# Kernel tuning notes

Hardware: AMD Instinct MI355X
Metric: run time of the kernel (lower is better)

Reference implementation:

```python
import jax, jax.numpy as jnp
import numpy as np

HIDDEN = 2048
HEADS = 16
HEAD_DIM = HIDDEN // HEADS
ROPE_BASE = 10000.0


def rope_cos_sin(seq_len, dim, dtype=jnp.float32):
    inv_freq = 1.0 / (ROPE_BASE ** (jnp.arange(0, dim, 2, dtype=jnp.float32) / dim))
    t = jnp.arange(seq_len, dtype=jnp.float32)
    freqs = jnp.einsum('i,j->ij', t, inv_freq)            # [S, dim/2]
    emb = jnp.concatenate([freqs, freqs], axis=-1)        # [S, dim]
    return jnp.cos(emb).astype(dtype), jnp.sin(emb).astype(dtype)


def rotate_half(x):
    x1, x2 = jnp.split(x, 2, axis=-1)
    return jnp.concatenate([-x2, x1], axis=-1)


def setup_inputs() -> dict:
    key = jax.random.key(0)
    ks = jax.random.split(key, 6)
    B, S, D = 2, 2048, HIDDEN
    scale = 1.0 / np.sqrt(D)
    x = jax.random.normal(ks[0], (B, S, D), dtype=jnp.float32)
    Wq = jax.random.normal(ks[1], (D, D), dtype=jnp.float32) * scale
    Wk = jax.random.normal(ks[2], (D, D), dtype=jnp.float32) * scale
    Wv = jax.random.normal(ks[3], (D, D), dtype=jnp.float32) * scale
    Wo = jax.random.normal(ks[4], (D, D), dtype=jnp.float32) * scale
    bo = jnp.zeros((D,), dtype=jnp.float32)
    return {"x": x, "Wq": Wq, "Wk": Wk, "Wv": Wv, "Wo": Wo, "bo": bo}


def reference(x, Wq, Wk, Wv, Wo, bo):
    B, S, D = x.shape
    H, Dh = HEADS, HEAD_DIM
    # torch Linear: x @ W.T
    q = (x @ Wq.T).reshape(B, S, H, Dh).transpose(0, 2, 1, 3)  # [B,H,S,Dh]
    k = (x @ Wk.T).reshape(B, S, H, Dh).transpose(0, 2, 1, 3)
    v = (x @ Wv.T).reshape(B, S, H, Dh).transpose(0, 2, 1, 3)
    cos, sin = rope_cos_sin(S, Dh, x.dtype)                    # [S, Dh]
    q = q * cos + rotate_half(q) * sin
    k = k * cos + rotate_half(k) * sin
    scale = Dh ** -0.5
    attn = jnp.einsum('bhqd,bhkd->bhqk', q, k) * scale
    attn = jax.nn.softmax(attn, axis=-1)
    out = jnp.einsum('bhqk,bhkd->bhqd', attn, v)               # [B,H,S,Dh]
    out = out.transpose(0, 2, 1, 3).reshape(B, S, D)
    return out @ Wo.T + bo
```

## Files before the change

kernel.cpp:

```cpp
#include <hip/hip_runtime.h>
#include <stdint.h>


#define SEQ 2048
#define HD 128
#define DMODEL 2048

typedef __bf16 bf16x8 __attribute__((ext_vector_type(8)));
typedef float f32x4 __attribute__((ext_vector_type(4)));
typedef unsigned short u16;
typedef unsigned int u32;

typedef bf16x8 __attribute__((may_alias)) bf16x8_a;
typedef uint2 __attribute__((may_alias)) uint2_a;
typedef uint4 __attribute__((may_alias)) uint4_a;

__device__ __forceinline__ u16 f2bf(float f) {
  unsigned int u = __float_as_uint(f);
  u += 0x7fff + ((u >> 16) & 1);
  return (u16)(u >> 16);
}

typedef __attribute__((address_space(1))) void* gas_t;
typedef __attribute__((address_space(3))) void* las_t;
__device__ __forceinline__ void load_lds16(const void* g, void* l) {
  __builtin_amdgcn_global_load_lds((gas_t)(uintptr_t)g,
                                   (las_t)(uint32_t)(uintptr_t)l, 16, 0, 0);
}

__global__ void conv_all(const float* __restrict__ x,
                         const float* __restrict__ wq,
                         const float* __restrict__ wk,
                         const float* __restrict__ wv,
                         const float* __restrict__ wo,
                         u16* __restrict__ xb, u16* __restrict__ wqkv,
                         u16* __restrict__ wob) {
  int i = blockIdx.x * 256 + threadIdx.x;
  const float* src;
  u16* dst;
  int off;
  if (i < 2097152) { src = x; dst = xb; off = i; }
  else if (i < 3145728) { src = wq; dst = wqkv; off = i - 2097152; }
  else if (i < 4194304) { src = wk; dst = wqkv + 4194304; off = i - 3145728; }
  else if (i < 5242880) { src = wv; dst = wqkv + 8388608; off = i - 4194304; }
  else { src = wo; dst = wob; off = i - 5242880; }
  float4 v = ((const float4*)src)[off];
  ushort4 o;
  o.x = f2bf(v.x); o.y = f2bf(v.y); o.z = f2bf(v.z); o.w = f2bf(v.w);
  ((ushort4*)dst)[off] = o;
}

template <bool SWAP>
__device__ __forceinline__ void gemm_core(
    const u16* __restrict__ A, const u16* __restrict__ Bm, int row0, int col0,
    int K, u16* Asl, u16* Bsl, int wave, int lane, int quad, int l15,
    int waveM, int waveN, f32x4 acc[4][4]) {
  for (int k0 = 0; k0 < K; k0 += 64) {
    __syncthreads();
#pragma unroll
    for (int j = 0; j < 4; ++j) {
      int idx = (wave * 4 + j) * 64 + lane;
      int r = idx >> 3;
      int c8 = (idx & 7) ^ (r & 7);
      load_lds16(A + (size_t)(row0 + r) * K + (k0 + c8 * 8), &Asl[idx * 8]);
      load_lds16(Bm + (size_t)(col0 + r) * K + (k0 + c8 * 8), &Bsl[idx * 8]);
    }
    __syncthreads();
#pragma unroll
    for (int c = 0; c < 2; ++c) {
      bf16x8 af[4], bfr[4];
#pragma unroll
      for (int mt = 0; mt < 4; ++mt) {
        int r = waveM + mt * 16 + l15;
        af[mt] = *(const bf16x8*)&Asl[(r * 8 + ((c * 4 + quad) ^ (r & 7))) * 8];
      }
#pragma unroll
      for (int nt = 0; nt < 4; ++nt) {
        int r = waveN + nt * 16 + l15;
        bfr[nt] = *(const bf16x8*)&Bsl[(r * 8 + ((c * 4 + quad) ^ (r & 7))) * 8];
      }
#pragma unroll
      for (int mt = 0; mt < 4; ++mt)
#pragma unroll
        for (int nt = 0; nt < 4; ++nt) {
          if (SWAP)
            acc[mt][nt] = __builtin_amdgcn_mfma_f32_16x16x32_bf16(
                bfr[nt], af[mt], acc[mt][nt], 0, 0, 0);
          else
            acc[mt][nt] = __builtin_amdgcn_mfma_f32_16x16x32_bf16(
                af[mt], bfr[nt], acc[mt][nt], 0, 0, 0);
        }
    }
  }
}

__global__ __launch_bounds__(256, 3)
void gemm_qkv(const u16* __restrict__ A, const u16* __restrict__ Bm,
              u16* __restrict__ qkv, u16* __restrict__ vt, int K) {
  __shared__ __align__(16) u16 Smem[2][128 * 64];
  u16* Asl = Smem[0];
  u16* Bsl = Smem[1];
  const int tid = threadIdx.x;
  const int lane = tid & 63;
  const int wave = tid >> 6;
  const int quad = lane >> 4;
  const int l15 = lane & 15;
  const int row0 = blockIdx.y * 128;
  const int col0 = blockIdx.x * 128;
  const int waveM = (wave & 1) * 64;
  const int waveN = (wave >> 1) * 64;
  const bool vmode = blockIdx.x >= 32;

  f32x4 acc[4][4] = {};
  if (vmode)
    gemm_core<true>(A, Bm, row0, col0, K, Asl, Bsl, wave, lane, quad, l15,
                    waveM, waveN, acc);
  else
    gemm_core<false>(A, Bm, row0, col0, K, Asl, Bsl, wave, lane, quad, l15,
                     waveM, waveN, acc);

  const int which = col0 >> 11;
  const int h = (col0 >> 7) & 15;
  const int brow = row0 >> 11;
  const int sbase = row0 & 2047;
  const float qs = (which == 0) ? 0.12751744f : 1.0f;

  __syncthreads();
  u16* tile = &Smem[0][0];
#pragma unroll
  for (int mt = 0; mt < 4; ++mt) {
#pragma unroll
    for (int nt = 0; nt < 4; ++nt) {
#pragma unroll
      for (int r = 0; r < 4; ++r) {
        int dd, ss, el;
        if (vmode) {
          dd = waveN + nt * 16 + quad * 4 + r;
          ss = waveM + mt * 16 + l15;
          el = dd * 128 + (((ss >> 3) ^ (dd & 15)) * 8) + (ss & 7);
        } else {
          dd = waveN + nt * 16 + l15;
          ss = waveM + mt * 16 + quad * 4 + r;
          el = ss * 128 + (((dd >> 3) ^ (ss & 15)) * 8) + (dd & 7);
        }
        tile[el] = f2bf(acc[mt][nt][r] * qs);
      }
    }
  }
  __syncthreads();

  const int a = lane & 7;
  const int sg = lane >> 3;
  if (!vmode) {
    const float c1 = 0.2076205059304601f;
    const float c2 = 2.6514961294723187f;
#pragma unroll
    for (int pass = 0; pass < 4; ++pass) {
      int s_l = pass * 32 + wave * 8 + sg;
      int sw = s_l & 15;
      bf16x8 x1 = *(const bf16x8_a*)&tile[s_l * 128 + ((a ^ sw) * 8)];
      bf16x8 x2 = *(const bf16x8_a*)&tile[s_l * 128 + (((a + 8) ^ sw) * 8)];
      int s2048 = sbase + s_l;
      u16 o1[8], o2[8];
#pragma unroll
      for (int e = 0; e < 8; ++e) {
        float j = (float)(a * 8 + e);
        float rev = (float)s2048 * __builtin_amdgcn_exp2f(-c1 * j - c2);
        rev = __builtin_amdgcn_fractf(rev);
        float sn = __builtin_amdgcn_sinf(rev);
        float cs = __builtin_amdgcn_cosf(rev);
        float v1 = (float)x1[e], v2 = (float)x2[e];
        o1[e] = f2bf(v1 * cs - v2 * sn);
        o2[e] = f2bf(v2 * cs + v1 * sn);
      }
      size_t base =
          ((((size_t)which * 2 + brow) * 16 + h) * SEQ + s2048) * HD + a * 8;
      *(uint4_a*)&qkv[base] = *(uint4*)o1;
      *(uint4_a*)&qkv[base + 64] = *(uint4*)o2;
    }
  } else {
#pragma unroll
    for (int pass = 0; pass < 4; ++pass) {
      int d_l = pass * 32 + wave * 8 + sg;
      int dw = d_l & 15;
      bf16x8 y1 = *(const bf16x8_a*)&tile[d_l * 128 + ((a ^ dw) * 8)];
      bf16x8 y2 = *(const bf16x8_a*)&tile[d_l * 128 + (((a + 8) ^ dw) * 8)];
      size_t base =
          (((size_t)brow * 16 + h) * HD + d_l) * SEQ + sbase + a * 8;
      *(uint4_a*)&vt[base] = *(uint4_a*)&y1;
      *(uint4_a*)&vt[base + 64] = *(uint4_a*)&y2;
    }
  }
}

__global__ __launch_bounds__(256, 3)
void gemm_out(const u16* __restrict__ A, const u16* __restrict__ Bm,
              float* __restrict__ C, const float* __restrict__ bias, int N,
              int K) {
  __shared__ __align__(16) u16 Smem[2][128 * 64];
  const int tid = threadIdx.x;
  const int lane = tid & 63;
  const int wave = tid >> 6;
  const int quad = lane >> 4;
  const int l15 = lane & 15;
  const int row0 = blockIdx.y * 128;
  const int col0 = blockIdx.x * 128;
  const int waveM = (wave & 1) * 64;
  const int waveN = (wave >> 1) * 64;

  f32x4 acc[4][4] = {};
  gemm_core<false>(A, Bm, row0, col0, K, Smem[0], Smem[1], wave, lane, quad,
                   l15, waveM, waveN, acc);

#pragma unroll
  for (int nt = 0; nt < 4; ++nt) {
    int d = col0 + waveN + nt * 16 + l15;
    float bv = bias[d];
#pragma unroll
    for (int mt = 0; mt < 4; ++mt) {
#pragma unroll
      for (int r = 0; r < 4; ++r) {
        int row = row0 + waveM + mt * 16 + quad * 4 + r;
        C[(size_t)row * N + d] = acc[mt][nt][r] + bv;
      }
    }
  }
}

__global__ __launch_bounds__(256, 2)
void attn_kernel(const u16* __restrict__ qkv, const u16* __restrict__ vt,
                 u16* __restrict__ attn_out) {
  __shared__ __align__(16) u16 Kl[64 * 128];
  __shared__ __align__(16) u16 Vl[128 * 64];
  __shared__ __align__(16) u16 Pl[4][32 * 64];

  const int tid = threadIdx.x;
  const int lane = tid & 63;
  const int wave = tid >> 6;
  const int quad = lane >> 4;
  const int l15 = lane & 15;
  const int q0 = blockIdx.x * 128;
  const int bh = blockIdx.y;
  const size_t SD = (size_t)SEQ * HD;

  const u16* Q = qkv + (size_t)bh * SD;
  const u16* Kg = qkv + (size_t)(32 + bh) * SD;
  const u16* Vg = vt + (size_t)bh * SD;

  bf16x8 onesf;
#pragma unroll
  for (int e = 0; e < 8; ++e)
    onesf[e] = (l15 == 0) ? (__bf16)1.0f : (__bf16)0.0f;

  bf16x8 qf[2][4];
#pragma unroll
  for (int mt = 0; mt < 2; ++mt) {
    int qrow = q0 + wave * 32 + mt * 16 + l15;
#pragma unroll
    for (int c = 0; c < 4; ++c)
      qf[mt][c] = *(const bf16x8*)(Q + (size_t)qrow * HD + c * 32 + quad * 8);
  }

  f32x4 of[9][2] = {};
  u16* pw = &Pl[wave][0];

  for (int kv0 = 0; kv0 < SEQ; kv0 += 64) {
    __syncthreads();
#pragma unroll
    for (int j = 0; j < 4; ++j) {
      int idx = (wave * 4 + j) * 64 + lane;
      {
        int r = idx >> 4, cs = idx & 15;
        int cc = cs ^ (r & 15);
        load_lds16(Kg + (size_t)(kv0 + r) * HD + cc * 8, &Kl[idx * 8]);
      }
      {
        int r = idx >> 3, cs = idx & 7;
        int cc = cs ^ (r & 7);
        load_lds16(Vg + (size_t)r * SEQ + kv0 + cc * 8, &Vl[idx * 8]);
      }
    }
    __syncthreads();

    f32x4 sc[4][2] = {};
#pragma unroll
    for (int c = 0; c < 4; ++c) {
      bf16x8 kf[4];
#pragma unroll
      for (int nt = 0; nt < 4; ++nt)
        kf[nt] = *(const bf16x8*)&Kl[((nt * 16 + l15) * 16 +
                                      ((c * 4 + quad) ^ l15)) * 8];
#pragma unroll
      for (int nt = 0; nt < 4; ++nt)
#pragma unroll
        for (int mt = 0; mt < 2; ++mt)
          sc[nt][mt] = __builtin_amdgcn_mfma_f32_16x16x32_bf16(
              kf[nt], qf[mt][c], sc[nt][mt], 0, 0, 0);
    }

#pragma unroll
    for (int nt = 0; nt < 4; ++nt) {
#pragma unroll
      for (int mt = 0; mt < 2; ++mt) {
        float p0 = __builtin_amdgcn_exp2f(sc[nt][mt][0]);
        float p1 = __builtin_amdgcn_exp2f(sc[nt][mt][1]);
        float p2 = __builtin_amdgcn_exp2f(sc[nt][mt][2]);
        float p3 = __builtin_amdgcn_exp2f(sc[nt][mt][3]);
        u32 lo = __builtin_amdgcn_perm(__float_as_uint(p1),
                                       __float_as_uint(p0), 0x07060302u);
        u32 hi = __builtin_amdgcn_perm(__float_as_uint(p3),
                                       __float_as_uint(p2), 0x07060302u);
        int row = mt * 16 + l15;
        int a = nt * 2 + (quad >> 1);
        int idx16 = (row * 8 + (a ^ (l15 & 7))) * 8 + (quad & 1) * 4;
        uint2 pk; pk.x = lo; pk.y = hi;
        *(uint2_a*)&pw[idx16] = pk;
      }
    }

#pragma unroll
    for (int c = 0; c < 2; ++c) {
      bf16x8 pf[2];
#pragma unroll
      for (int mt = 0; mt < 2; ++mt)
        pf[mt] = *(const bf16x8_a*)&pw[((mt * 16 + l15) * 8 +
                                        ((c * 4 + quad) ^ (l15 & 7))) * 8];
#pragma unroll
      for (int dt = 0; dt < 9; ++dt) {
        bf16x8 vf = (dt < 8)
                        ? *(const bf16x8*)&Vl[((dt * 16 + l15) * 8 +
                                               ((c * 4 + quad) ^ (l15 & 7))) * 8]
                        : onesf;
#pragma unroll
        for (int mt = 0; mt < 2; ++mt)
          of[dt][mt] = __builtin_amdgcn_mfma_f32_16x16x32_bf16(
              vf, pf[mt], of[dt][mt], 0, 0, 0);
      }
    }
  }

  const int b = bh >> 4, h = bh & 15;
#pragma unroll
  for (int mt = 0; mt < 2; ++mt) {
    float lsum = __shfl(of[8][mt][0], l15, 64);
    float inv = 1.f / lsum;
    int s = q0 + wave * 32 + mt * 16 + l15;
    size_t rowb = ((size_t)b * SEQ + s) * DMODEL + h * HD;
#pragma unroll
    for (int dt = 0; dt < 8; ++dt) {
      ushort4 ov;
      ov.x = f2bf(of[dt][mt][0] * inv);
      ov.y = f2bf(of[dt][mt][1] * inv);
      ov.z = f2bf(of[dt][mt][2] * inv);
      ov.w = f2bf(of[dt][mt][3] * inv);
      *(ushort4*)&attn_out[rowb + dt * 16 + quad * 4] = ov;
    }
  }
}

extern "C" void kernel_launch(void* const* d_in, const int* in_sizes, int n_in,
                              void* d_out, int out_size, void* d_ws,
                              size_t ws_size, hipStream_t stream) {
  const float* x = (const float*)d_in[0];
  const float* Wq = (const float*)d_in[1];
  const float* Wk = (const float*)d_in[2];
  const float* Wv = (const float*)d_in[3];
  const float* Wo = (const float*)d_in[4];
  const float* bo = (const float*)d_in[5];
  float* out = (float*)d_out;

  char* ws = (char*)d_ws;
  u16* xb = (u16*)(ws);
  u16* wqkv = (u16*)(ws + (size_t)(16 << 20));
  u16* wob = (u16*)(ws + (size_t)(40 << 20));
  u16* qkv = (u16*)(ws + (size_t)(48 << 20));
  u16* vt = qkv + (size_t)2 * 8388608;
  u16* attn = xb;

  conv_all<<<24576, 256, 0, stream>>>(x, Wq, Wk, Wv, Wo, xb, wqkv, wob);

  gemm_qkv<<<dim3(48, 32), 256, 0, stream>>>(xb, wqkv, qkv, vt, 2048);
  attn_kernel<<<dim3(16, 32), 256, 0, stream>>>(qkv, vt, attn);
  gemm_out<<<dim3(16, 32), 256, 0, stream>>>(attn, wob, out, bo, 2048, 2048);
}
```

Baseline: 375.5 us.

## Rewrite QKV GEMM as 256x256 tiles with 8-wave ping-pong LDS pipeline

Replaces the 128x128, 4-wave QKV projection GEMM with a 256x256 tile, 512-thread kernel. Staging is a hand-scheduled double-buffered global-to-LDS pipeline with explicit barriers, waitcnts and setprio around the MFMA clusters. It also adds a grid swizzle for L2 locality and widens the RoPE and V-transpose epilogue to cover two heads per block. The aim is to raise arithmetic intensity and overlap loads with MFMA work, at the cost of 128KB LDS per block, fewer blocks (384) and a fragile manual synchronisation schedule.

Result: no change. 373.3 us (-0.6%).

```diff
diff --git a/kernel.cpp b/kernel.cpp
--- a/kernel.cpp
+++ b/kernel.cpp
@@ -94,101 +94,230 @@
   }
 }
 
-__global__ __launch_bounds__(256, 3)
-void gemm_qkv(const u16* __restrict__ A, const u16* __restrict__ Bm,
-              u16* __restrict__ qkv, u16* __restrict__ vt, int K) {
-  __shared__ __align__(16) u16 Smem[2][128 * 64];
-  u16* Asl = Smem[0];
-  u16* Bsl = Smem[1];
-  const int tid = threadIdx.x;
+
+#define BARR asm volatile("s_barrier" ::: "memory")
+#define LGKM0 asm volatile("s_waitcnt lgkmcnt(0)" ::: "memory")
+#define VMW4 asm volatile("s_waitcnt vmcnt(4)" ::: "memory")
+#define VMW0 asm volatile("s_waitcnt vmcnt(0)" ::: "memory")
+
+#define STG(OP, DB, HF, KOFF) do {                                          \
+    const u16* gb_ = ((OP) ? Bg : Ag) + (HF) * 262144 + (KOFF);             \
+    u16* lb_ = S + ((OP) ? 32768 : 0) + (DB) * 16384 + (HF) * 8192;         \
+    load_lds16(gb_ + off0, lb_ + tid * 8);                                  \
+    load_lds16(gb_ + off1, lb_ + (tid + 512) * 8);                          \
+  } while (0)
+
+#define LDA(DB, MH) do {                                                    \
+    const u16* ab_ = S + (DB) * 16384 + wm * 8192;                          \
+    _Pragma("unroll") for (int mt_ = 0; mt_ < 4; ++mt_) {                   \
+      int rA_ = (MH) * 64 + mt_ * 16 + l15;                                 \
+      int sw_ = rA_ & 7;                                                    \
+      af[mt_][0] = *(const bf16x8_a*)(ab_ + (rA_ * 8 + (quad ^ sw_)) * 8);  \
+      af[mt_][1] = *(const bf16x8_a*)(ab_ + (rA_ * 8 + ((4 + quad) ^ sw_)) * 8); \
+    } } while (0)
+
+#define LDB(DB, NH, DST) do {                                               \
+    const u16* bb_ = S + 32768 + (DB) * 16384 + (wn >> 1) * 8192;           \
+    _Pragma("unroll") for (int nt_ = 0; nt_ < 2; ++nt_) {                   \
+      int rB_ = (wn & 1) * 64 + (NH) * 32 + nt_ * 16 + l15;                 \
+      int sw_ = rB_ & 7;                                                    \
+      DST[nt_][0] = *(const bf16x8_a*)(bb_ + (rB_ * 8 + (quad ^ sw_)) * 8); \
+      DST[nt_][1] = *(const bf16x8_a*)(bb_ + (rB_ * 8 + ((4 + quad) ^ sw_)) * 8); \
+    } } while (0)
+
+#define MMQ(MH, NH, BFR) do {                                               \
+    __builtin_amdgcn_s_setprio(1);                                          \
+    _Pragma("unroll") for (int c_ = 0; c_ < 2; ++c_)                        \
+      _Pragma("unroll") for (int mt_ = 0; mt_ < 4; ++mt_)                   \
+        _Pragma("unroll") for (int nt_ = 0; nt_ < 2; ++nt_) {               \
+          if (VM)                                                           \
+            acc[(MH) * 4 + mt_][(NH) * 2 + nt_] =                           \
+                __builtin_amdgcn_mfma_f32_16x16x32_bf16(                    \
+                    BFR[nt_][c_], af[mt_][c_],                              \
+                    acc[(MH) * 4 + mt_][(NH) * 2 + nt_], 0, 0, 0);          \
+          else                                                              \
+            acc[(MH) * 4 + mt_][(NH) * 2 + nt_] =                           \
+                __builtin_amdgcn_mfma_f32_16x16x32_bf16(                    \
+                    af[mt_][c_], BFR[nt_][c_],                              \
+                    acc[(MH) * 4 + mt_][(NH) * 2 + nt_], 0, 0, 0);          \
+        }                                                                   \
+    __builtin_amdgcn_s_setprio(0);                                          \
+  } while (0)
+
+template <bool VM>
+__device__ __forceinline__ void qkv_core(const u16* __restrict__ Ag,
+                                         const u16* __restrict__ Bg,
+                                         u16* __restrict__ S, int tid,
+                                         f32x4 acc[8][4]) {
   const int lane = tid & 63;
   const int wave = tid >> 6;
   const int quad = lane >> 4;
   const int l15 = lane & 15;
-  const int row0 = blockIdx.y * 128;
-  const int col0 = blockIdx.x * 128;
-  const int waveM = (wave & 1) * 64;
-  const int waveN = (wave >> 1) * 64;
-  const bool vmode = blockIdx.x >= 32;
-
-  f32x4 acc[4][4] = {};
-  if (vmode)
-    gemm_core<true>(A, Bm, row0, col0, K, Asl, Bsl, wave, lane, quad, l15,
-                    waveM, waveN, acc);
-  else
-    gemm_core<false>(A, Bm, row0, col0, K, Asl, Bsl, wave, lane, quad, l15,
-                     waveM, waveN, acc);
+  const int wm = wave >> 2;
+  const int wn = wave & 3;
+
+  const int r0_ = tid >> 3;
+  const u32 off0 = (u32)r0_ * 2048u + (u32)(((tid & 7) ^ (r0_ & 7)) * 8);
+  const int i1_ = tid + 512;
+  const int r1_ = i1_ >> 3;
+  const u32 off1 = (u32)r1_ * 2048u + (u32)(((i1_ & 7) ^ (r1_ & 7)) * 8);
+
+  bf16x8 af[4][2], bn0[2][2], bn1[2][2];
+
+  STG(1, 0, 0, 0);
+  STG(0, 0, 0, 0);
+  STG(0, 0, 1, 0);
+  STG(1, 0, 1, 0);
+  STG(1, 1, 0, 64);
+  STG(1, 1, 1, 64);
+  VMW4;
+  BARR;
+
+#pragma unroll 1
+  for (int kb = 0; kb < 1920; kb += 128) {
+    LDA(0, 0); LDB(0, 0, bn0); STG(0, 1, 0, kb + 64);
+    BARR; LGKM0; MMQ(0, 0, bn0); BARR;
+    LDB(0, 1, bn1); STG(0, 1, 1, kb + 64);
+    BARR; LGKM0; MMQ(0, 1, bn1); BARR;
+    LDA(0, 1); STG(1, 0, 0, kb + 128);
+    BARR; LGKM0; MMQ(1, 0, bn0); BARR;
+    STG(0, 0, 0, kb + 128);
+    BARR; MMQ(1, 1, bn1); VMW4; BARR;
+    LDA(1, 0); LDB(1, 0, bn0); STG(0, 0, 1, kb + 128);
+    BARR; LGKM0; MMQ(0, 0, bn0); BARR;
+    LDB(1, 1, bn1); STG(1, 0, 1, kb + 128);
+    BARR; LGKM0; MMQ(0, 1, bn1); BARR;
+    LDA(1, 1); STG(1, 1, 0, kb + 192);
+    BARR; LGKM0; MMQ(1, 0, bn0); BARR;
+    STG(1, 1, 1, kb + 192);
+    BARR; MMQ(1, 1, bn1); VMW4; BARR;
+  }
+
+  LDA(0, 0); LDB(0, 0, bn0); STG(0, 1, 0, 1984);
+  BARR; LGKM0; MMQ(0, 0, bn0); BARR;
+  LDB(0, 1, bn1); STG(0, 1, 1, 1984);
+  BARR; LGKM0; MMQ(0, 1, bn1); BARR;
+  LDA(0, 1);
+  BARR; LGKM0; MMQ(1, 0, bn0); BARR;
+  BARR; MMQ(1, 1, bn1); VMW0; BARR;
+  LDA(1, 0); LDB(1, 0, bn0);
+  BARR; LGKM0; MMQ(0, 0, bn0); BARR;
+  LDB(1, 1, bn1);
+  BARR; LGKM0; MMQ(0, 1, bn1); BARR;
+  LDA(1, 1);
+  BARR; LGKM0; MMQ(1, 0, bn0); BARR;
+  BARR; MMQ(1, 1, bn1); BARR;
+}
+
+#undef STG
+#undef LDA
+#undef LDB
+#undef MMQ
+
+__global__ __launch_bounds__(512, 2)
+void gemm_qkv(const u16* __restrict__ A, const u16* __restrict__ Bm,
+              u16* __restrict__ qkv, u16* __restrict__ vt) {
+  __shared__ __align__(16) u16 S[65536];
+
+  const int tid = threadIdx.x;
+  int orig = blockIdx.y * 24 + blockIdx.x;
+  int swz = (orig & 7) * 48 + (orig >> 3);
+  const int bx = swz % 24;
+  const int by = swz / 24;
+  const int row0 = by * 256;
+  const int col0 = bx * 256;
+  const bool vmode = bx >= 16;
+
+  const u16* Ag = A + (size_t)row0 * 2048;
+  const u16* Bg = Bm + (size_t)col0 * 2048;
+
+  f32x4 acc[8][4] = {};
+  if (vmode) qkv_core<true>(Ag, Bg, S, tid, acc);
+  else       qkv_core<false>(Ag, Bg, S, tid, acc);
+
+  const int lane = tid & 63;
+  const int wave = tid >> 6;
+  const int quad = lane >> 4;
+  const int l15 = lane & 15;
+  const int wm = wave >> 2;
+  const int wn = wave & 3;
 
   const int which = col0 >> 11;
-  const int h = (col0 >> 7) & 15;
+  const float qs = (which == 0) ? 0.12751744f : 1.0f;
+
+#pragma unroll
+  for (int mh = 0; mh < 2; ++mh)
+#pragma unroll
+    for (int nh = 0; nh < 2; ++nh)
+#pragma unroll
+      for (int mt = 0; mt < 4; ++mt)
+#pragma unroll
+        for (int nt = 0; nt < 2; ++nt)
+#pragma unroll
+          for (int r = 0; r < 4; ++r) {
+            int el;
+            if (vmode) {
+              int dd = wn * 64 + nh * 32 + nt * 16 + quad * 4 + r;
+              int ss = wm * 128 + mh * 64 + mt * 16 + l15;
+              el = dd * 256 + (((ss >> 3) ^ (dd & 31)) * 8) + (ss & 7);
+            } else {
+              int ss = wm * 128 + mh * 64 + mt * 16 + quad * 4 + r;
+              int dd = wn * 64 + nh * 32 + nt * 16 + l15;
+              el = ss * 256 + (((dd >> 3) ^ (ss & 31)) * 8) + (dd & 7);
+            }
+            S[el] = f2bf(acc[mh * 4 + mt][nh * 2 + nt][r] * qs);
+          }
+  __syncthreads();
+
+  const int a = lane & 7;
+  const int sg = lane >> 3;
+  const int h0 = (col0 >> 7) & 15;
   const int brow = row0 >> 11;
   const int sbase = row0 & 2047;
-  const float qs = (which == 0) ? 0.12751744f : 1.0f;
-
-  __syncthreads();
-  u16* tile = &Smem[0][0];
-#pragma unroll
-  for (int mt = 0; mt < 4; ++mt) {
-#pragma unroll
-    for (int nt = 0; nt < 4; ++nt) {
-#pragma unroll
-      for (int r = 0; r < 4; ++r) {
-        int dd, ss, el;
-        if (vmode) {
-          dd = waveN + nt * 16 + quad * 4 + r;
-          ss = waveM + mt * 16 + l15;
-          el = dd * 128 + (((ss >> 3) ^ (dd & 15)) * 8) + (ss & 7);
-        } else {
-          dd = waveN + nt * 16 + l15;
-          ss = waveM + mt * 16 + quad * 4 + r;
-          el = ss * 128 + (((dd >> 3) ^ (ss & 15)) * 8) + (dd & 7);
-        }
-        tile[el] = f2bf(acc[mt][nt][r] * qs);
-      }
-    }
-  }
-  __syncthreads();
-
-  const int a = lane & 7;
-  const int sg = lane >> 3;
+
   if (!vmode) {
     const float c1 = 0.2076205059304601f;
     const float c2 = 2.6514961294723187f;
 #pragma unroll
     for (int pass = 0; pass < 4; ++pass) {
-      int s_l = pass * 32 + wave * 8 + sg;
-      int sw = s_l & 15;
-      bf16x8 x1 = *(const bf16x8_a*)&tile[s_l * 128 + ((a ^ sw) * 8)];
-      bf16x8 x2 = *(const bf16x8_a*)&tile[s_l * 128 + (((a + 8) ^ sw) * 8)];
+      int s_l = pass * 64 + wave * 8 + sg;
       int s2048 = sbase + s_l;
-      u16 o1[8], o2[8];
-#pragma unroll
-      for (int e = 0; e < 8; ++e) {
-        float j = (float)(a * 8 + e);
-        float rev = (float)s2048 * __builtin_amdgcn_exp2f(-c1 * j - c2);
-        rev = __builtin_amdgcn_fractf(rev);
-        float sn = __builtin_amdgcn_sinf(rev);
-        float cs = __builtin_amdgcn_cosf(rev);
-        float v1 = (float)x1[e], v2 = (float)x2[e];
-        o1[e] = f2bf(v1 * cs - v2 * sn);
-        o2[e] = f2bf(v2 * cs + v1 * sn);
-      }
-      size_t base =
-          ((((size_t)which * 2 + brow) * 16 + h) * SEQ + s2048) * HD + a * 8;
-      *(uint4_a*)&qkv[base] = *(uint4*)o1;
-      *(uint4_a*)&qkv[base + 64] = *(uint4*)o2;
+      int sw = s_l & 31;
+#pragma unroll
+      for (int hh = 0; hh < 2; ++hh) {
+        bf16x8 x1 = *(const bf16x8_a*)&S[s_l * 256 + (((hh * 16 + a) ^ sw) * 8)];
+        bf16x8 x2 = *(const bf16x8_a*)&S[s_l * 256 + (((hh * 16 + a + 8) ^ sw) * 8)];
+        u16 o1[8], o2[8];
+#pragma unroll
+        for (int e = 0; e < 8; ++e) {
+          float j = (float)(a * 8 + e);
+          float rev = (float)s2048 * __builtin_amdgcn_exp2f(-c1 * j - c2);
+          rev = __builtin_amdgcn_fractf(rev);
+          float sn = __builtin_amdgcn_sinf(rev);
+          float cs = __builtin_amdgcn_cosf(rev);
+          float v1 = (float)x1[e], v2 = (float)x2[e];
+          o1[e] = f2bf(v1 * cs - v2 * sn);
+          o2[e] = f2bf(v2 * cs + v1 * sn);
+        }
+        size_t base = ((((size_t)which * 2 + brow) * 16 + (h0 + hh)) * SEQ +
+                       s2048) * HD + a * 8;
+        *(uint4_a*)&qkv[base] = *(uint4*)o1;
+        *(uint4_a*)&qkv[base + 64] = *(uint4*)o2;
+      }
     }
   } else {
 #pragma unroll
     for (int pass = 0; pass < 4; ++pass) {
-      int d_l = pass * 32 + wave * 8 + sg;
-      int dw = d_l & 15;
-      bf16x8 y1 = *(const bf16x8_a*)&tile[d_l * 128 + ((a ^ dw) * 8)];
-      bf16x8 y2 = *(const bf16x8_a*)&tile[d_l * 128 + (((a + 8) ^ dw) * 8)];
-      size_t base =
-          (((size_t)brow * 16 + h) * HD + d_l) * SEQ + sbase + a * 8;
-      *(uint4_a*)&vt[base] = *(uint4_a*)&y1;
-      *(uint4_a*)&vt[base + 64] = *(uint4_a*)&y2;
+      int d_l = pass * 64 + wave * 8 + sg;
+      int h = h0 + (d_l >> 7);
+      int dw = d_l & 31;
+      size_t rb = (((size_t)brow * 16 + h) * HD + (d_l & 127)) * SEQ + sbase;
+#pragma unroll
+      for (int g = 0; g < 4; ++g) {
+        int As = g * 8 + a;
+        bf16x8 y = *(const bf16x8_a*)&S[d_l * 256 + ((As ^ dw) * 8)];
+        *(uint4_a*)&vt[rb + As * 8] = *(uint4_a*)&y;
+      }
     }
   }
 }
@@ -379,7 +508,7 @@
 
   conv_all<<<24576, 256, 0, stream>>>(x, Wq, Wk, Wv, Wo, xb, wqkv, wob);
 
-  gemm_qkv<<<dim3(48, 32), 256, 0, stream>>>(xb, wqkv, qkv, vt, 2048);
+  gemm_qkv<<<dim3(24, 16), 512, 0, stream>>>(xb, wqkv, qkv, vt);
   attn_kernel<<<dim3(16, 32), 256, 0, stream>>>(qkv, vt, attn);
   gemm_out<<<dim3(16, 32), 256, 0, stream>>>(attn, wob, out, bo, 2048, 2048);
 }
```

## Pipeline GEMM and attention loads with double-buffered LDS and larger tiles

Applied to the files above, without the earlier changes.

Rewrites the GEMM core as a 256x128 tile with 512 threads, double-buffered LDS staging that keeps global loads in flight across k-steps under manual vmcnt waits, and MFMA priority boosts. It also remaps block IDs into an XCD-aware order to improve L2 reuse. The attention kernel gains double-buffered K/V tiles prefetched two steps ahead. The aim is to hide global-load latency and cut barrier stalls, at the cost of more LDS per block, lower occupancy and fragile hand-placed wait counts.

After: 358.9 us. 1.05x faster.

```diff
diff --git a/kernel.cpp b/kernel.cpp
--- a/kernel.cpp
+++ b/kernel.cpp
@@ -50,117 +50,174 @@
   ((ushort4*)dst)[off] = o;
 }
 
-template <bool SWAP>
-__device__ __forceinline__ void gemm_core(
-    const u16* __restrict__ A, const u16* __restrict__ Bm, int row0, int col0,
-    int K, u16* Asl, u16* Bsl, int wave, int lane, int quad, int l15,
-    int waveM, int waveN, f32x4 acc[4][4]) {
-  for (int k0 = 0; k0 < K; k0 += 64) {
-    __syncthreads();
-#pragma unroll
-    for (int j = 0; j < 4; ++j) {
-      int idx = (wave * 4 + j) * 64 + lane;
-      int r = idx >> 3;
-      int c8 = (idx & 7) ^ (r & 7);
-      load_lds16(A + (size_t)(row0 + r) * K + (k0 + c8 * 8), &Asl[idx * 8]);
-      load_lds16(Bm + (size_t)(col0 + r) * K + (k0 + c8 * 8), &Bsl[idx * 8]);
-    }
-    __syncthreads();
-#pragma unroll
-    for (int c = 0; c < 2; ++c) {
-      bf16x8 af[4], bfr[4];
-#pragma unroll
-      for (int mt = 0; mt < 4; ++mt) {
-        int r = waveM + mt * 16 + l15;
-        af[mt] = *(const bf16x8*)&Asl[(r * 8 + ((c * 4 + quad) ^ (r & 7))) * 8];
-      }
-#pragma unroll
-      for (int nt = 0; nt < 4; ++nt) {
-        int r = waveN + nt * 16 + l15;
-        bfr[nt] = *(const bf16x8*)&Bsl[(r * 8 + ((c * 4 + quad) ^ (r & 7))) * 8];
-      }
-#pragma unroll
-      for (int mt = 0; mt < 4; ++mt)
-#pragma unroll
-        for (int nt = 0; nt < 4; ++nt) {
-          if (SWAP)
-            acc[mt][nt] = __builtin_amdgcn_mfma_f32_16x16x32_bf16(
-                bfr[nt], af[mt], acc[mt][nt], 0, 0, 0);
-          else
-            acc[mt][nt] = __builtin_amdgcn_mfma_f32_16x16x32_bf16(
-                af[mt], bfr[nt], acc[mt][nt], 0, 0, 0);
-        }
-    }
-  }
-}
-
-__global__ __launch_bounds__(256, 3)
-void gemm_qkv(const u16* __restrict__ A, const u16* __restrict__ Bm,
-              u16* __restrict__ qkv, u16* __restrict__ vt, int K) {
-  __shared__ __align__(16) u16 Smem[2][128 * 64];
-  u16* Asl = Smem[0];
-  u16* Bsl = Smem[1];
-  const int tid = threadIdx.x;
+
+#define BARR asm volatile("s_barrier" ::: "memory")
+#define LGKM0 asm volatile("s_waitcnt lgkmcnt(0)" ::: "memory")
+#define VMW2 asm volatile("s_waitcnt vmcnt(2)" ::: "memory")
+#define VMW8 asm volatile("s_waitcnt vmcnt(8)" ::: "memory")
+#define VMW0 asm volatile("s_waitcnt vmcnt(0)" ::: "memory")
+
+#define STGA(D, KOFF) do {                                                  \
+    const u16* ga_ = Ag + (KOFF);                                           \
+    u16* la_ = S + (D) * 16384;                                             \
+    load_lds16(ga_ + off[0], la_ + tid * 8);                                \
+    load_lds16(ga_ + off[1], la_ + (tid + 512) * 8);                        \
+    load_lds16(ga_ + off[2], la_ + (tid + 1024) * 8);                       \
+    load_lds16(ga_ + off[3], la_ + (tid + 1536) * 8);                       \
+  } while (0)
+
+#define STGB(D, KOFF) do {                                                  \
+    const u16* gb_ = Bg + (KOFF);                                           \
+    u16* lb_ = S + 32768 + (D) * 8192;                                      \
+    load_lds16(gb_ + off[0], lb_ + tid * 8);                                \
+    load_lds16(gb_ + off[1], lb_ + (tid + 512) * 8);                        \
+  } while (0)
+
+#define LDA2(D, MH) do {                                                    \
+    const u16* ab_ = S + (D) * 16384;                                       \
+    _Pragma("unroll") for (int mt_ = 0; mt_ < 2; ++mt_) {                   \
+      int rA_ = wm * 64 + ((MH) * 2 + mt_) * 16 + l15;                      \
+      int sw_ = rA_ & 7;                                                    \
+      af[mt_][0] = *(const bf16x8_a*)(ab_ + (rA_ * 8 + (quad ^ sw_)) * 8);  \
+      af[mt_][1] = *(const bf16x8_a*)(ab_ + (rA_ * 8 + ((4 + quad) ^ sw_)) * 8); \
+    } } while (0)
+
+#define LDB2(D) do {                                                        \
+    const u16* bb_ = S + 32768 + (D) * 8192;                                \
+    _Pragma("unroll") for (int nt_ = 0; nt_ < 4; ++nt_) {                   \
+      int rB_ = wn * 64 + nt_ * 16 + l15;                                   \
+      int sw_ = rB_ & 7;                                                    \
+      bfr[nt_][0] = *(const bf16x8_a*)(bb_ + (rB_ * 8 + (quad ^ sw_)) * 8); \
+      bfr[nt_][1] = *(const bf16x8_a*)(bb_ + (rB_ * 8 + ((4 + quad) ^ sw_)) * 8); \
+    } } while (0)
+
+#define MM2(MH) do {                                                        \
+    __builtin_amdgcn_s_setprio(1);                                          \
+    _Pragma("unroll") for (int c_ = 0; c_ < 2; ++c_)                        \
+      _Pragma("unroll") for (int mt_ = 0; mt_ < 2; ++mt_)                   \
+        _Pragma("unroll") for (int nt_ = 0; nt_ < 4; ++nt_) {               \
+          if (VM)                                                           \
+            acc[(MH) * 2 + mt_][nt_] =                                      \
+                __builtin_amdgcn_mfma_f32_16x16x32_bf16(                    \
+                    bfr[nt_][c_], af[mt_][c_],                              \
+                    acc[(MH) * 2 + mt_][nt_], 0, 0, 0);                     \
+          else                                                              \
+            acc[(MH) * 2 + mt_][nt_] =                                      \
+                __builtin_amdgcn_mfma_f32_16x16x32_bf16(                    \
+                    af[mt_][c_], bfr[nt_][c_],                              \
+                    acc[(MH) * 2 + mt_][nt_], 0, 0, 0);                     \
+        }                                                                   \
+    __builtin_amdgcn_s_setprio(0);                                          \
+  } while (0)
+
+template <bool VM>
+__device__ __forceinline__ void mm_core(const u16* __restrict__ Ag,
+                                        const u16* __restrict__ Bg,
+                                        u16* __restrict__ S, int tid,
+                                        f32x4 acc[4][4]) {
   const int lane = tid & 63;
   const int wave = tid >> 6;
   const int quad = lane >> 4;
   const int l15 = lane & 15;
-  const int row0 = blockIdx.y * 128;
-  const int col0 = blockIdx.x * 128;
-  const int waveM = (wave & 1) * 64;
-  const int waveN = (wave >> 1) * 64;
-  const bool vmode = blockIdx.x >= 32;
+  const int wm = wave >> 1;
+  const int wn = wave & 1;
+
+  u32 off[4];
+#pragma unroll
+  for (int j = 0; j < 4; ++j) {
+    int idx = tid + j * 512;
+    int r = idx >> 3;
+    off[j] = (u32)r * 2048u + (u32)(((idx & 7) ^ (r & 7)) * 8);
+  }
+
+  bf16x8 af[2][2], bfr[4][2];
+
+  STGA(0, 0);
+  STGB(0, 0);
+  STGB(1, 64);
+  VMW2;
+  BARR;
+
+#pragma unroll 2
+  for (int t = 0; t < 32; ++t) {
+    const int d = t & 1;
+    LDA2(d, 0); LDB2(d);
+    if (t < 31) STGA(1 - d, (t + 1) * 64);
+    BARR; LGKM0; MM2(0); BARR;
+    LDA2(d, 1);
+    if (t < 30) STGB(d, (t + 2) * 64);
+    BARR; LGKM0; MM2(1);
+    if (t < 30) { VMW2; } else if (t == 30) { VMW0; }
+    BARR;
+  }
+}
+
+__global__ __launch_bounds__(512, 2)
+void gemm_qkv(const u16* __restrict__ A, const u16* __restrict__ Bm,
+              u16* __restrict__ qkv, u16* __restrict__ vt) {
+  __shared__ __align__(16) u16 S[49152];
+
+  const int tid = threadIdx.x;
+  int hwid = blockIdx.y * 48 + blockIdx.x;
+  int logical = (hwid & 7) * 96 + (hwid >> 3);
+  const int bx = logical >> 4;
+  const int by = logical & 15;
+  const int row0 = by * 256;
+  const int col0 = bx * 128;
+  const bool vmode = bx >= 32;
+
+  const u16* Ag = A + (size_t)row0 * 2048;
+  const u16* Bg = Bm + (size_t)col0 * 2048;
 
   f32x4 acc[4][4] = {};
-  if (vmode)
-    gemm_core<true>(A, Bm, row0, col0, K, Asl, Bsl, wave, lane, quad, l15,
-                    waveM, waveN, acc);
-  else
-    gemm_core<false>(A, Bm, row0, col0, K, Asl, Bsl, wave, lane, quad, l15,
-                     waveM, waveN, acc);
-
-  const int which = col0 >> 11;
-  const int h = (col0 >> 7) & 15;
+  if (vmode) mm_core<true>(Ag, Bg, S, tid, acc);
+  else       mm_core<false>(Ag, Bg, S, tid, acc);
+
+  const int lane = tid & 63;
+  const int wave = tid >> 6;
+  const int quad = lane >> 4;
+  const int l15 = lane & 15;
+  const int wm = wave >> 1;
+  const int wn = wave & 1;
+
+  const int which = bx >> 4;
+  const int h = bx & 15;
   const int brow = row0 >> 11;
   const int sbase = row0 & 2047;
   const float qs = (which == 0) ? 0.12751744f : 1.0f;
 
-  __syncthreads();
-  u16* tile = &Smem[0][0];
-#pragma unroll
-  for (int mt = 0; mt < 4; ++mt) {
-#pragma unroll
-    for (int nt = 0; nt < 4; ++nt) {
+#pragma unroll
+  for (int mt = 0; mt < 4; ++mt)
+#pragma unroll
+    for (int nt = 0; nt < 4; ++nt)
 #pragma unroll
       for (int r = 0; r < 4; ++r) {
-        int dd, ss, el;
+        int el;
         if (vmode) {
-          dd = waveN + nt * 16 + quad * 4 + r;
-          ss = waveM + mt * 16 + l15;
-          el = dd * 128 + (((ss >> 3) ^ (dd & 15)) * 8) + (ss & 7);
+          int dd = wn * 64 + nt * 16 + quad * 4 + r;
+          int ss = wm * 64 + mt * 16 + l15;
+          el = dd * 256 + (((ss >> 3) ^ (dd & 31)) * 8) + (ss & 7);
         } else {
-          dd = waveN + nt * 16 + l15;
-          ss = waveM + mt * 16 + quad * 4 + r;
+          int ss = wm * 64 + mt * 16 + quad * 4 + r;
+          int dd = wn * 64 + nt * 16 + l15;
           el = ss * 128 + (((dd >> 3) ^ (ss & 15)) * 8) + (dd & 7);
         }
-        tile[el] = f2bf(acc[mt][nt][r] * qs);
-      }
-    }
-  }
+        S[el] = f2bf(acc[mt][nt][r] * qs);
+      }
   __syncthreads();
 
-  const int a = lane & 7;
-  const int sg = lane >> 3;
   if (!vmode) {
+    const int a = lane & 7;
+    const int sg = lane >> 3;
     const float c1 = 0.2076205059304601f;
     const float c2 = 2.6514961294723187f;
 #pragma unroll
     for (int pass = 0; pass < 4; ++pass) {
-      int s_l = pass * 32 + wave * 8 + sg;
+      int s_l = pass * 64 + wave * 8 + sg;
+      int s2048 = sbase + s_l;
       int sw = s_l & 15;
-      bf16x8 x1 = *(const bf16x8_a*)&tile[s_l * 128 + ((a ^ sw) * 8)];
-      bf16x8 x2 = *(const bf16x8_a*)&tile[s_l * 128 + (((a + 8) ^ sw) * 8)];
-      int s2048 = sbase + s_l;
+      bf16x8 x1 = *(const bf16x8_a*)&S[s_l * 128 + ((a ^ sw) * 8)];
+      bf16x8 x2 = *(const bf16x8_a*)&S[s_l * 128 + (((a + 8) ^ sw) * 8)];
       u16 o1[8], o2[8];
 #pragma unroll
       for (int e = 0; e < 8; ++e) {
@@ -179,49 +236,59 @@
       *(uint4_a*)&qkv[base + 64] = *(uint4*)o2;
     }
   } else {
+    const int d_part = tid >> 4;
+    const int a0 = tid & 15;
 #pragma unroll
     for (int pass = 0; pass < 4; ++pass) {
-      int d_l = pass * 32 + wave * 8 + sg;
-      int dw = d_l & 15;
-      bf16x8 y1 = *(const bf16x8_a*)&tile[d_l * 128 + ((a ^ dw) * 8)];
-      bf16x8 y2 = *(const bf16x8_a*)&tile[d_l * 128 + (((a + 8) ^ dw) * 8)];
-      size_t base =
-          (((size_t)brow * 16 + h) * HD + d_l) * SEQ + sbase + a * 8;
-      *(uint4_a*)&vt[base] = *(uint4_a*)&y1;
-      *(uint4_a*)&vt[base + 64] = *(uint4_a*)&y2;
-    }
-  }
-}
-
-__global__ __launch_bounds__(256, 3)
+      int d_l = pass * 32 + d_part;
+      int dw = d_l & 31;
+      size_t rb = (((size_t)brow * 16 + h) * HD + d_l) * SEQ + sbase;
+#pragma unroll
+      for (int g = 0; g < 2; ++g) {
+        int a2 = a0 + g * 16;
+        bf16x8 y = *(const bf16x8_a*)&S[d_l * 256 + ((a2 ^ dw) * 8)];
+        *(uint4_a*)&vt[rb + a2 * 8] = *(uint4_a*)&y;
+      }
+    }
+  }
+}
+
+__global__ __launch_bounds__(512, 2)
 void gemm_out(const u16* __restrict__ A, const u16* __restrict__ Bm,
-              float* __restrict__ C, const float* __restrict__ bias, int N,
-              int K) {
-  __shared__ __align__(16) u16 Smem[2][128 * 64];
+              float* __restrict__ C, const float* __restrict__ bias) {
+  __shared__ __align__(16) u16 S[49152];
+
   const int tid = threadIdx.x;
+  int hwid = blockIdx.y * 16 + blockIdx.x;
+  int logical = (hwid & 7) * 32 + (hwid >> 3);
+  const int bx = logical >> 4;
+  const int by = logical & 15;
+  const int row0 = by * 256;
+  const int col0 = bx * 128;
+
+  const u16* Ag = A + (size_t)row0 * 2048;
+  const u16* Bg = Bm + (size_t)col0 * 2048;
+
+  f32x4 acc[4][4] = {};
+  mm_core<false>(Ag, Bg, S, tid, acc);
+
   const int lane = tid & 63;
   const int wave = tid >> 6;
   const int quad = lane >> 4;
   const int l15 = lane & 15;
-  const int row0 = blockIdx.y * 128;
-  const int col0 = blockIdx.x * 128;
-  const int waveM = (wave & 1) * 64;
-  const int waveN = (wave >> 1) * 64;
-
-  f32x4 acc[4][4] = {};
-  gemm_core<false>(A, Bm, row0, col0, K, Smem[0], Smem[1], wave, lane, quad,
-                   l15, waveM, waveN, acc);
+  const int wm = wave >> 1;
+  const int wn = wave & 1;
 
 #pragma unroll
   for (int nt = 0; nt < 4; ++nt) {
-    int d = col0 + waveN + nt * 16 + l15;
+    int d = col0 + wn * 64 + nt * 16 + l15;
     float bv = bias[d];
 #pragma unroll
     for (int mt = 0; mt < 4; ++mt) {
 #pragma unroll
       for (int r = 0; r < 4; ++r) {
-        int row = row0 + waveM + mt * 16 + quad * 4 + r;
-        C[(size_t)row * N + d] = acc[mt][nt][r] + bv;
+        int row = row0 + wm * 64 + mt * 16 + quad * 4 + r;
+        C[(size_t)row * DMODEL + d] = acc[mt][nt][r] + bv;
       }
     }
   }
@@ -230,8 +297,8 @@
 __global__ __launch_bounds__(256, 2)
 void attn_kernel(const u16* __restrict__ qkv, const u16* __restrict__ vt,
                  u16* __restrict__ attn_out) {
-  __shared__ __align__(16) u16 Kl[64 * 128];
-  __shared__ __align__(16) u16 Vl[128 * 64];
+  __shared__ __align__(16) u16 Kl[2][64 * 128];
+  __shared__ __align__(16) u16 Vl[2][128 * 64];
   __shared__ __align__(16) u16 Pl[4][32 * 64];
 
   const int tid = threadIdx.x;
@@ -264,31 +331,42 @@
   f32x4 of[9][2] = {};
   u16* pw = &Pl[wave][0];
 
-  for (int kv0 = 0; kv0 < SEQ; kv0 += 64) {
-    __syncthreads();
+  auto stage = [&](int tile, int buf) {
+    int kv0 = tile * 64;
 #pragma unroll
     for (int j = 0; j < 4; ++j) {
       int idx = (wave * 4 + j) * 64 + lane;
       {
         int r = idx >> 4, cs = idx & 15;
         int cc = cs ^ (r & 15);
-        load_lds16(Kg + (size_t)(kv0 + r) * HD + cc * 8, &Kl[idx * 8]);
+        load_lds16(Kg + (size_t)(kv0 + r) * HD + cc * 8, &Kl[buf][idx * 8]);
       }
       {
         int r = idx >> 3, cs = idx & 7;
         int cc = cs ^ (r & 7);
-        load_lds16(Vg + (size_t)r * SEQ + kv0 + cc * 8, &Vl[idx * 8]);
-      }
-    }
-    __syncthreads();
+        load_lds16(Vg + (size_t)r * SEQ + kv0 + cc * 8, &Vl[buf][idx * 8]);
+      }
+    }
+  };
+
+  stage(0, 0);
+  stage(1, 1);
+  VMW8;
+  BARR;
+
+#pragma unroll 2
+  for (int t = 0; t < 32; ++t) {
+    const u16* Kb = Kl[t & 1];
+    const u16* Vb = Vl[t & 1];
 
     f32x4 sc[4][2] = {};
+    __builtin_amdgcn_s_setprio(1);
 #pragma unroll
     for (int c = 0; c < 4; ++c) {
       bf16x8 kf[4];
 #pragma unroll
       for (int nt = 0; nt < 4; ++nt)
-        kf[nt] = *(const bf16x8*)&Kl[((nt * 16 + l15) * 16 +
+        kf[nt] = *(const bf16x8*)&Kb[((nt * 16 + l15) * 16 +
                                       ((c * 4 + quad) ^ l15)) * 8];
 #pragma unroll
       for (int nt = 0; nt < 4; ++nt)
@@ -297,6 +375,7 @@
           sc[nt][mt] = __builtin_amdgcn_mfma_f32_16x16x32_bf16(
               kf[nt], qf[mt][c], sc[nt][mt], 0, 0, 0);
     }
+    __builtin_amdgcn_s_setprio(0);
 
 #pragma unroll
     for (int nt = 0; nt < 4; ++nt) {
@@ -318,6 +397,7 @@
       }
     }
 
+    __builtin_amdgcn_s_setprio(1);
 #pragma unroll
     for (int c = 0; c < 2; ++c) {
       bf16x8 pf[2];
@@ -328,7 +408,7 @@
 #pragma unroll
       for (int dt = 0; dt < 9; ++dt) {
         bf16x8 vf = (dt < 8)
-                        ? *(const bf16x8*)&Vl[((dt * 16 + l15) * 8 +
+                        ? *(const bf16x8*)&Vb[((dt * 16 + l15) * 8 +
                                                ((c * 4 + quad) ^ (l15 & 7))) * 8]
                         : onesf;
 #pragma unroll
@@ -337,6 +417,16 @@
               vf, pf[mt], of[dt][mt], 0, 0, 0);
       }
     }
+    __builtin_amdgcn_s_setprio(0);
+
+    BARR;
+    if (t < 30) {
+      stage(t + 2, t & 1);
+      VMW8;
+    } else {
+      VMW0;
+    }
+    BARR;
   }
 
   const int b = bh >> 4, h = bh & 15;
@@ -379,7 +469,7 @@
 
   conv_all<<<24576, 256, 0, stream>>>(x, Wq, Wk, Wv, Wo, xb, wqkv, wob);
 
-  gemm_qkv<<<dim3(48, 32), 256, 0, stream>>>(xb, wqkv, qkv, vt, 2048);
+  gemm_qkv<<<dim3(48, 16), 512, 0, stream>>>(xb, wqkv, qkv, vt);
   attn_kernel<<<dim3(16, 32), 256, 0, stream>>>(qkv, vt, attn);
-  gemm_out<<<dim3(16, 32), 256, 0, stream>>>(attn, wob, out, bo, 2048, 2048);
-}
+  gemm_out<<<dim3(16, 16), 512, 0, stream>>>(attn, wob, out, bo);
+}
```
